# Kernel tuning notes

Hardware: AMD Instinct MI355X
Metric: run time of the kernel (lower is better)

Reference implementation:

```python
import jax, jax.numpy as jnp
import numpy as np

D = 1024
H = 16
HD = D // H


def setup_inputs() -> dict:
    key = jax.random.key(0)
    ks = jax.random.split(key, 9)
    s = 1.0 / np.sqrt(D)
    x = jax.random.normal(ks[0], (2, 2048, D), dtype=jnp.float32)
    Wq = jax.random.uniform(ks[1], (D, D), jnp.float32, -s, s)
    bq = jax.random.uniform(ks[2], (D,), jnp.float32, -s, s)
    Wk = jax.random.uniform(ks[3], (D, D), jnp.float32, -s, s)
    bk = jax.random.uniform(ks[4], (D,), jnp.float32, -s, s)
    Wv = jax.random.uniform(ks[5], (D, D), jnp.float32, -s, s)
    bv = jax.random.uniform(ks[6], (D,), jnp.float32, -s, s)
    Wo = jax.random.uniform(ks[7], (D, D), jnp.float32, -s, s)
    bo = jax.random.uniform(ks[8], (D,), jnp.float32, -s, s)
    return {"x": x, "Wq": Wq, "bq": bq, "Wk": Wk, "bk": bk,
            "Wv": Wv, "bv": bv, "Wo": Wo, "bo": bo}


def reference(x, Wq, bq, Wk, bk, Wv, bv, Wo, bo):
    B, S, _ = x.shape
    # project and split heads -> [B, H, S, HD]
    def split(t):
        return t.reshape(B, S, H, HD).transpose(0, 2, 1, 3)
    q = split(x @ Wq + bq)
    k = split(x @ Wk + bk)
    v = split(x @ Wv + bv)
    scores = jnp.einsum('bhqd,bhkd->bhqk', q, k) / np.sqrt(HD).astype(np.float32)
    attn = jax.nn.softmax(scores, axis=-1)
    ctx = jnp.einsum('bhqk,bhkd->bhqd', attn, v)  # [B,H,S,HD]
    ctx = ctx.transpose(0, 2, 1, 3).reshape(B, S, D)
    return ctx @ Wo + bo
```

## Files before the change

### kernel.cpp

```cpp
#include <hip/hip_runtime.h>
#include <hip/hip_bf16.h>
#include <math.h>

#define BB 2
#define SS 2048
#define DD 1024
#define HH 16
#define HD 64
#define MM (BB * SS)
#define NT (SS / 64)

typedef __bf16 bf16;
typedef __attribute__((ext_vector_type(8))) __bf16 bf16x8;
typedef __attribute__((ext_vector_type(4))) __bf16 bf16x4;
typedef __attribute__((ext_vector_type(4))) float f32x4;
typedef __attribute__((ext_vector_type(4))) unsigned u32x4;

#define QSCL 0.18033688011112042f

__device__ __forceinline__ void glds16(const bf16* g, bf16* l) {
    __builtin_amdgcn_global_load_lds(
        (const __attribute__((address_space(1))) void*)g,
        (__attribute__((address_space(3))) void*)l, 16, 0, 0);
}

__device__ __forceinline__ unsigned cvtpk_bf16(float a, float b) {
    unsigned r;
    asm("v_cvt_pk_bf16_f32 %0, %1, %2" : "=v"(r) : "v"(a), "v"(b));
    return r;
}

__device__ __forceinline__ float exp2p(float s) {
    float n = rintf(s);
    float f = s - n;
    float p = fmaf(f, 0.00961812910f, 0.0555041087f);
    p = fmaf(f, p, 0.240226507f);
    p = fmaf(f, p, 0.693147180f);
    p = fmaf(f, p, 1.0f);
    return ldexpf(p, (int)n);
}

__global__ __launch_bounds__(256) void cvt_prep(
    const float* __restrict__ x, bf16* __restrict__ xb,
    const float* __restrict__ W0, const float* __restrict__ W1,
    const float* __restrict__ W2, const float* __restrict__ W3,
    bf16* __restrict__ Wt) {
    __shared__ float T[64][65];
    const int bid = blockIdx.x;
    if (bid < 4096) {
        int i = (bid * 256 + threadIdx.x) * 4;
        float4 v = *(const float4*)(x + i);
        bf16x4 o;
        o[0] = (bf16)v.x; o[1] = (bf16)v.y; o[2] = (bf16)v.z; o[3] = (bf16)v.w;
        *(bf16x4*)(xb + i) = o;
        return;
    }
    const int b = bid - 4096;
    const int z = b >> 8;
    const float* W = (z == 0) ? W0 : (z == 1) ? W1 : (z == 2) ? W2 : W3;
    bf16* dst = Wt + (size_t)z * DD * DD;
    int k0 = ((b >> 4) & 15) * 64, n0 = (b & 15) * 64;
    int tr = threadIdx.x >> 4, tc = (threadIdx.x & 15) * 4;
#pragma unroll
    for (int u = 0; u < 4; u++) {
        int r = tr + u * 16;
        float4 v = *(const float4*)&W[(size_t)(k0 + r) * DD + n0 + tc];
        T[tc + 0][r] = v.x; T[tc + 1][r] = v.y;
        T[tc + 2][r] = v.z; T[tc + 3][r] = v.w;
    }
    __syncthreads();
#pragma unroll
    for (int u = 0; u < 4; u++) {
        int r = tr + u * 16;
        bf16x4 o;
        o[0] = (bf16)T[r][tc + 0]; o[1] = (bf16)T[r][tc + 1];
        o[2] = (bf16)T[r][tc + 2]; o[3] = (bf16)T[r][tc + 3];
        *(bf16x4*)&dst[(size_t)(n0 + r) * DD + k0 + tc] = o;
    }
}

__global__ __launch_bounds__(256) void mfma_gemm(
    const bf16* __restrict__ A, const bf16* __restrict__ Wt0,
    const float* __restrict__ b0, const float* __restrict__ b1,
    const float* __restrict__ b2,
    bf16* __restrict__ o0, bf16* __restrict__ o1, bf16* __restrict__ o2) {
    const int lin = blockIdx.x;
    const int nl = (lin & 7) * 96 + (lin >> 3);
    const int z = nl >> 8;
    const int rem = nl & 255;
    const int m0 = (rem >> 3) * 128;
    const int n0 = (rem & 7) * 128;

    const bf16* Wt = Wt0 + (size_t)z * DD * DD;
    const float* bias = (z == 0) ? b0 : (z == 1) ? b1 : b2;
    const float scl = (z == 0) ? QSCL : 1.0f;

    __shared__ __align__(16) bf16 As[128 * 64];
    __shared__ __align__(16) bf16 Bs[128 * 64];

    const int tid = threadIdx.x;
    const int lane = tid & 63;
    const int w = tid >> 6;
    const int l15 = lane & 15, quad = lane >> 4;
    const int mw = (w & 1) * 64;
    const int nw = (w >> 1) * 64;

    f32x4 acc[4][4];
#pragma unroll
    for (int i = 0; i < 4; i++)
#pragma unroll
        for (int j = 0; j < 4; j++) acc[i][j] = (f32x4){0.f, 0.f, 0.f, 0.f};

    for (int kt = 0; kt < DD; kt += 64) {
        __syncthreads();
#pragma unroll
        for (int u = 0; u < 4; u++) {
            int j = tid + u * 256;
            int row = j >> 3, cp = j & 7;
            int c = cp ^ (row & 7);
            glds16(A  + (size_t)(m0 + row) * DD + kt + c * 8, &As[j * 8]);
            glds16(Wt + (size_t)(n0 + row) * DD + kt + c * 8, &Bs[j * 8]);
        }
        __syncthreads();

#pragma unroll
        for (int kh = 0; kh < 2; kh++) {
            bf16x8 af[4], bf[4];
#pragma unroll
            for (int i = 0; i < 4; i++) {
                int ra = mw + i * 16 + l15;
                int ja = ra * 8 + ((kh * 4 + quad) ^ (ra & 7));
                af[i] = *(const bf16x8*)&As[ja * 8];
                int rb = nw + i * 16 + l15;
                int jb = rb * 8 + ((kh * 4 + quad) ^ (rb & 7));
                bf[i] = *(const bf16x8*)&Bs[jb * 8];
            }
#pragma unroll
            for (int i = 0; i < 4; i++)
#pragma unroll
                for (int j = 0; j < 4; j++)
                    acc[i][j] = __builtin_amdgcn_mfma_f32_16x16x32_bf16(
                        af[i], bf[j], acc[i][j], 0, 0, 0);
        }
    }

    float bcol[4];
#pragma unroll
    for (int j = 0; j < 4; j++) bcol[j] = bias[n0 + nw + j * 16 + l15];

    if (z == 2) {
        const int mbase = m0 + mw;
        const int bb = (mbase >= SS) ? 1 : 0;
        const int sw = mbase & (SS - 1);
#pragma unroll
        for (int i = 0; i < 4; i++) {
            int scol = sw + (i >> 1) * 32 + quad * 8 + (i & 1) * 4;
#pragma unroll
            for (int j = 0; j < 4; j++) {
                int dg = n0 + nw + j * 16 + l15;
                int h = dg >> 6, d = dg & 63;
                bf16* dst = o2 + ((size_t)(bb * HH + h) * HD + d) * SS + scol;
                bf16x4 ov;
#pragma unroll
                for (int r = 0; r < 4; r++)
                    ov[r] = (bf16)(acc[i][j][r] + bcol[j]);
                *(bf16x4*)dst = ov;
            }
        }
    } else {
        bf16* dstb = (z == 0) ? o0 : o1;
#pragma unroll
        for (int i = 0; i < 4; i++)
#pragma unroll
            for (int j = 0; j < 4; j++)
#pragma unroll
                for (int r = 0; r < 4; r++) {
                    int row = m0 + mw + i * 16 + quad * 4 + r;
                    int col = n0 + nw + j * 16 + l15;
                    dstb[(size_t)row * DD + col] =
                        (bf16)((acc[i][j][r] + bcol[j]) * scl);
                }
    }
}

__global__ __launch_bounds__(256) void mfma_gemm_out(
    const bf16* __restrict__ A, const bf16* __restrict__ Wt,
    const float* __restrict__ bias, float* __restrict__ out) {
    const int lin = blockIdx.x;
    const int nl = (lin & 7) * 64 + (lin >> 3);
    const int m0 = (nl >> 3) * 64;
    const int n0 = (nl & 7) * 128;

    __shared__ __align__(16) bf16 As[64 * 64];
    __shared__ __align__(16) bf16 Bs[128 * 64];

    const int tid = threadIdx.x;
    const int lane = tid & 63;
    const int w = tid >> 6;
    const int l15 = lane & 15, quad = lane >> 4;
    const int mw = (w & 1) * 32;
    const int nw = (w >> 1) * 64;

    f32x4 acc[2][4];
#pragma unroll
    for (int i = 0; i < 2; i++)
#pragma unroll
        for (int j = 0; j < 4; j++) acc[i][j] = (f32x4){0.f, 0.f, 0.f, 0.f};

    for (int kt = 0; kt < DD; kt += 64) {
        __syncthreads();
#pragma unroll
        for (int u = 0; u < 2; u++) {
            int j = tid + u * 256;
            int row = j >> 3, c = (j & 7) ^ (row & 7);
            glds16(A + (size_t)(m0 + row) * DD + kt + c * 8, &As[j * 8]);
        }
#pragma unroll
        for (int u = 0; u < 4; u++) {
            int j = tid + u * 256;
            int row = j >> 3, c = (j & 7) ^ (row & 7);
            glds16(Wt + (size_t)(n0 + row) * DD + kt + c * 8, &Bs[j * 8]);
        }
        __syncthreads();

#pragma unroll
        for (int kh = 0; kh < 2; kh++) {
            bf16x8 af[2], bf[4];
#pragma unroll
            for (int i = 0; i < 2; i++) {
                int ra = mw + i * 16 + l15;
                int ja = ra * 8 + ((kh * 4 + quad) ^ (ra & 7));
                af[i] = *(const bf16x8*)&As[ja * 8];
            }
#pragma unroll
            for (int j = 0; j < 4; j++) {
                int rb = nw + j * 16 + l15;
                int jb = rb * 8 + ((kh * 4 + quad) ^ (rb & 7));
                bf[j] = *(const bf16x8*)&Bs[jb * 8];
            }
#pragma unroll
            for (int i = 0; i < 2; i++)
#pragma unroll
                for (int j = 0; j < 4; j++)
                    acc[i][j] = __builtin_amdgcn_mfma_f32_16x16x32_bf16(
                        af[i], bf[j], acc[i][j], 0, 0, 0);
        }
    }

    float bcol[4];
#pragma unroll
    for (int j = 0; j < 4; j++) bcol[j] = bias[n0 + nw + j * 16 + l15];

#pragma unroll
    for (int i = 0; i < 2; i++)
#pragma unroll
        for (int j = 0; j < 4; j++)
#pragma unroll
            for (int r = 0; r < 4; r++) {
                int row = m0 + mw + i * 16 + quad * 4 + r;
                int col = n0 + nw + j * 16 + l15;
                out[(size_t)row * DD + col] = acc[i][j][r] + bcol[j];
            }
}

__global__ __launch_bounds__(256) void mfma_attn(
    const bf16* __restrict__ Qb, const bf16* __restrict__ Kb,
    const bf16* __restrict__ Vtg, bf16* __restrict__ ctxb) {
    __shared__ __align__(16) bf16 Ks[2][64 * 64];
    __shared__ __align__(16) bf16 Vs[2][64 * 64];

    const int lin = blockIdx.x;
    const int nl = (lin & 7) * 128 + (lin >> 3);
    const int bh = nl >> 5;
    const int q0 = (nl & 31) * 64;

    const int tid = threadIdx.x;
    const int lane = tid & 63;
    const int w = tid >> 6;
    const int l15 = lane & 15, quad = lane >> 4;
    const int b = bh >> 4, h = bh & 15;
    const size_t mb = (size_t)b * SS;
    const int hc = h * HD;
    const bf16* Vt_bh = Vtg + (size_t)bh * HD * SS;

    bf16x8 qf[2];
#pragma unroll
    for (int kh = 0; kh < 2; kh++)
        qf[kh] = *(const bf16x8*)&Qb[(mb + q0 + w * 16 + l15) * DD +
                                     hc + kh * 32 + quad * 8];

    bf16x8 onev;
#pragma unroll
    for (int i = 0; i < 8; i++) onev[i] = (bf16)1.0f;
    const f32x4 zf = (f32x4){0.f, 0.f, 0.f, 0.f};

    int koff[4][2], voff[4][2];
#pragma unroll
    for (int kb = 0; kb < 4; kb++) {
        int rk = kb * 16 + l15;
#pragma unroll
        for (int kh = 0; kh < 2; kh++)
            koff[kb][kh] = (rk * 8 + ((kh * 4 + quad) ^ (rk & 7))) * 8;
    }
#pragma unroll
    for (int nb = 0; nb < 4; nb++) {
        int rv = nb * 16 + l15;
#pragma unroll
        for (int kh = 0; kh < 2; kh++)
            voff[nb][kh] = (rv * 8 + ((kh * 4 + quad) ^ (rv & 7))) * 8;
    }

    const bf16* gK[2]; const bf16* gV[2]; int lo_[2];
#pragma unroll
    for (int u = 0; u < 2; u++) {
        int j = tid + u * 256;
        int row = j >> 3, cp = j & 7;
        int c = cp ^ (row & 7);
        gK[u] = Kb + (mb + row) * DD + hc + c * 8;
        gV[u] = Vt_bh + (size_t)row * SS + c * 8;
        lo_[u] = j * 8;
    }

    f32x4 o[4], lsum;
    lsum = (f32x4){0.f, 0.f, 0.f, 0.f};
#pragma unroll
    for (int nb = 0; nb < 4; nb++) o[nb] = (f32x4){0.f, 0.f, 0.f, 0.f};

#pragma unroll
    for (int u = 0; u < 2; u++) {
        glds16(gK[u], &Ks[0][lo_[u]]);  gK[u] += 64 * DD;
        glds16(gV[u], &Vs[0][lo_[u]]);  gV[u] += 64;
    }
    __syncthreads();

    f32x4 scA[4];
#pragma unroll
    for (int kb = 0; kb < 4; kb++) {
        bf16x8 kf0 = *(const bf16x8*)&Ks[0][koff[kb][0]];
        bf16x8 kf1 = *(const bf16x8*)&Ks[0][koff[kb][1]];
        f32x4 t = __builtin_amdgcn_mfma_f32_16x16x32_bf16(
            kf0, qf[0], zf, 0, 0, 0);
        scA[kb] = __builtin_amdgcn_mfma_f32_16x16x32_bf16(
            kf1, qf[1], t, 0, 0, 0);
    }

    int buf = 0;
    for (int it = 0; it < NT; ++it) {
        const bool more = (it + 1 < NT);
        if (more) {
#pragma unroll
            for (int u = 0; u < 2; u++) {
                glds16(gK[u], &Ks[buf ^ 1][lo_[u]]);  gK[u] += 64 * DD;
                glds16(gV[u], &Vs[buf ^ 1][lo_[u]]);  gV[u] += 64;
            }
        }

        u32x4 pw[2];
#pragma unroll
        for (int kb = 0; kb < 4; kb++) {
            float p0 = exp2p(scA[kb][0]);
            float p1 = exp2p(scA[kb][1]);
            float p2 = exp2p(scA[kb][2]);
            float p3 = exp2p(scA[kb][3]);
            pw[kb >> 1][(kb & 1) * 2 + 0] = cvtpk_bf16(p0, p1);
            pw[kb >> 1][(kb & 1) * 2 + 1] = cvtpk_bf16(p2, p3);
        }
        bf16x8 pfr[2];
        pfr[0] = __builtin_bit_cast(bf16x8, pw[0]);
        pfr[1] = __builtin_bit_cast(bf16x8, pw[1]);

        __syncthreads();

        __builtin_amdgcn_s_setprio(1);
        f32x4 scB[4];
        if (more) {
#pragma unroll
            for (int kb = 0; kb < 4; kb++) {
                bf16x8 kf0 = *(const bf16x8*)&Ks[buf ^ 1][koff[kb][0]];
                bf16x8 kf1 = *(const bf16x8*)&Ks[buf ^ 1][koff[kb][1]];
                f32x4 t = __builtin_amdgcn_mfma_f32_16x16x32_bf16(
                    kf0, qf[0], zf, 0, 0, 0);
                scB[kb] = __builtin_amdgcn_mfma_f32_16x16x32_bf16(
                    kf1, qf[1], t, 0, 0, 0);
            }
        }
#pragma unroll
        for (int kh = 0; kh < 2; kh++) {
            lsum = __builtin_amdgcn_mfma_f32_16x16x32_bf16(
                pfr[kh], onev, lsum, 0, 0, 0);
#pragma unroll
            for (int nb = 0; nb < 4; nb++) {
                bf16x8 vf = *(const bf16x8*)&Vs[buf][voff[nb][kh]];
                o[nb] = __builtin_amdgcn_mfma_f32_16x16x32_bf16(
                    pfr[kh], vf, o[nb], 0, 0, 0);
            }
        }
        __builtin_amdgcn_s_setprio(0);

        __syncthreads();

        if (more) {
#pragma unroll
            for (int kb = 0; kb < 4; kb++) scA[kb] = scB[kb];
        }
        buf ^= 1;
    }

    float li[4];
#pragma unroll
    for (int r = 0; r < 4; r++) li[r] = 1.0f / lsum[r];
#pragma unroll
    for (int nb = 0; nb < 4; nb++)
#pragma unroll
        for (int r = 0; r < 4; r++) {
            int qrow = q0 + w * 16 + quad * 4 + r;
            ctxb[(mb + qrow) * DD + hc + nb * 16 + l15] =
                (bf16)(o[nb][r] * li[r]);
        }
}

extern "C" void kernel_launch(void* const* d_in, const int* in_sizes, int n_in,
                              void* d_out, int out_size, void* d_ws, size_t ws_size,
                              hipStream_t stream) {
    const float* x  = (const float*)d_in[0];
    const float* Wq = (const float*)d_in[1];
    const float* bq = (const float*)d_in[2];
    const float* Wk = (const float*)d_in[3];
    const float* bk = (const float*)d_in[4];
    const float* Wv = (const float*)d_in[5];
    const float* bv = (const float*)d_in[6];
    const float* Wo = (const float*)d_in[7];
    const float* bo = (const float*)d_in[8];
    float* out = (float*)d_out;

    char* base = (char*)d_ws;
    bf16* xb   = (bf16*)(base);
    bf16* Wt   = (bf16*)(base + (8ull  << 20));
    bf16* Qb   = (bf16*)(base + (16ull << 20));
    bf16* Kb   = (bf16*)(base + (24ull << 20));
    bf16* Vt   = (bf16*)(base + (32ull << 20));
    bf16* ctxb = (bf16*)(base + (40ull << 20));

    cvt_prep<<<dim3(4096 + 1024), dim3(256), 0, stream>>>(
        x, xb, Wq, Wk, Wv, Wo, Wt);

    mfma_gemm<<<dim3(768), dim3(256), 0, stream>>>(
        xb, Wt, bq, bk, bv, Qb, Kb, Vt);

    mfma_attn<<<dim3(1024), dim3(256), 0, stream>>>(Qb, Kb, Vt, ctxb);

    mfma_gemm_out<<<dim3(512), dim3(256), 0, stream>>>(
        ctxb, Wt + 3ull * DD * DD, bo, out);
}
```

Measured before the change: 208.4 us.

## Rework QKV GEMM into 256x256 tiles with double-buffered LDS prefetch

The fused QKV projection GEMM moves from 128x128 tiles with 256 threads to 256x256 tiles with 512 threads, each wave computing a 128x64 sub-tile. LDS is double-buffered so the next K-slice is loaded with global_load_lds while MFMAs run on the current one, with one barrier per iteration instead of two. The MFMA section also runs at raised wave priority. The grid drops to 192 blocks, under one wave of blocks across the CUs, and the 128 KB of LDS plus larger accumulators may limit occupancy.

Result: faster. 203.7 us (median of 2 runs) (-2.2%).

```diff
diff --git a/kernel.cpp b/kernel.cpp
--- a/kernel.cpp
+++ b/kernel.cpp
@@ -79,85 +79,106 @@
     }
 }
 
-__global__ __launch_bounds__(256) void mfma_gemm(
+__global__ __launch_bounds__(512, 2) void mfma_gemm_qkv(
     const bf16* __restrict__ A, const bf16* __restrict__ Wt0,
     const float* __restrict__ b0, const float* __restrict__ b1,
     const float* __restrict__ b2,
     bf16* __restrict__ o0, bf16* __restrict__ o1, bf16* __restrict__ o2) {
+    __shared__ __align__(16) bf16 As[2][256 * 64];
+    __shared__ __align__(16) bf16 Bs[2][256 * 64];
+
     const int lin = blockIdx.x;
-    const int nl = (lin & 7) * 96 + (lin >> 3);
-    const int z = nl >> 8;
-    const int rem = nl & 255;
-    const int m0 = (rem >> 3) * 128;
-    const int n0 = (rem & 7) * 128;
-
-    const bf16* Wt = Wt0 + (size_t)z * DD * DD;
+    const int nl = (lin & 7) * 24 + (lin >> 3);
+    const int mt = nl & 15;
+    const int nt = nl >> 4;
+    const int m0 = mt * 256;
+    const int n0g = nt * 256;
+    const int z = n0g >> 10;
+    const int n0 = n0g & 1023;
+    const bf16* Wt = Wt0 + (size_t)z * DD * DD + (size_t)n0 * DD;
     const float* bias = (z == 0) ? b0 : (z == 1) ? b1 : b2;
     const float scl = (z == 0) ? QSCL : 1.0f;
-
-    __shared__ __align__(16) bf16 As[128 * 64];
-    __shared__ __align__(16) bf16 Bs[128 * 64];
 
     const int tid = threadIdx.x;
     const int lane = tid & 63;
     const int w = tid >> 6;
+    const int wm = w >> 2;
+    const int wn = w & 3;
     const int l15 = lane & 15, quad = lane >> 4;
-    const int mw = (w & 1) * 64;
-    const int nw = (w >> 1) * 64;
-
-    f32x4 acc[4][4];
-#pragma unroll
-    for (int i = 0; i < 4; i++)
+
+    const bf16* gA[4]; const bf16* gB[4]; int loff[4];
+#pragma unroll
+    for (int u = 0; u < 4; u++) {
+        int j = tid + u * 512;
+        int r = j >> 3, cp = j & 7;
+        int c = cp ^ (r & 7);
+        gA[u] = A  + (size_t)(m0 + r) * DD + c * 8;
+        gB[u] = Wt + (size_t)r * DD + c * 8;
+        loff[u] = j * 8;
+    }
+
+    f32x4 acc[8][4];
+#pragma unroll
+    for (int i = 0; i < 8; i++)
 #pragma unroll
         for (int j = 0; j < 4; j++) acc[i][j] = (f32x4){0.f, 0.f, 0.f, 0.f};
 
-    for (int kt = 0; kt < DD; kt += 64) {
-        __syncthreads();
-#pragma unroll
-        for (int u = 0; u < 4; u++) {
-            int j = tid + u * 256;
-            int row = j >> 3, cp = j & 7;
-            int c = cp ^ (row & 7);
-            glds16(A  + (size_t)(m0 + row) * DD + kt + c * 8, &As[j * 8]);
-            glds16(Wt + (size_t)(n0 + row) * DD + kt + c * 8, &Bs[j * 8]);
-        }
-        __syncthreads();
-
+#pragma unroll
+    for (int u = 0; u < 4; u++) {
+        glds16(gA[u], &As[0][loff[u]]);  gA[u] += 64;
+        glds16(gB[u], &Bs[0][loff[u]]);  gB[u] += 64;
+    }
+    __syncthreads();
+
+    for (int t = 0; t < DD / 64; ++t) {
+        const int buf = t & 1;
+        if (t + 1 < DD / 64) {
+#pragma unroll
+            for (int u = 0; u < 4; u++) {
+                glds16(gA[u], &As[buf ^ 1][loff[u]]);  gA[u] += 64;
+                glds16(gB[u], &Bs[buf ^ 1][loff[u]]);  gB[u] += 64;
+            }
+        }
+        __builtin_amdgcn_s_setprio(1);
 #pragma unroll
         for (int kh = 0; kh < 2; kh++) {
-            bf16x8 af[4], bf[4];
-#pragma unroll
-            for (int i = 0; i < 4; i++) {
-                int ra = mw + i * 16 + l15;
-                int ja = ra * 8 + ((kh * 4 + quad) ^ (ra & 7));
-                af[i] = *(const bf16x8*)&As[ja * 8];
-                int rb = nw + i * 16 + l15;
-                int jb = rb * 8 + ((kh * 4 + quad) ^ (rb & 7));
-                bf[i] = *(const bf16x8*)&Bs[jb * 8];
-            }
-#pragma unroll
-            for (int i = 0; i < 4; i++)
+            bf16x8 bfr[4];
+#pragma unroll
+            for (int j = 0; j < 4; j++) {
+                int rb = wn * 64 + j * 16 + l15;
+                bfr[j] = *(const bf16x8*)
+                    &Bs[buf][rb * 64 + (((kh * 4 + quad) ^ (rb & 7)) << 3)];
+            }
+#pragma unroll
+            for (int i = 0; i < 8; i++) {
+                int ra = wm * 128 + i * 16 + l15;
+                bf16x8 afr = *(const bf16x8*)
+                    &As[buf][ra * 64 + (((kh * 4 + quad) ^ (ra & 7)) << 3)];
 #pragma unroll
                 for (int j = 0; j < 4; j++)
                     acc[i][j] = __builtin_amdgcn_mfma_f32_16x16x32_bf16(
-                        af[i], bf[j], acc[i][j], 0, 0, 0);
-        }
+                        afr, bfr[j], acc[i][j], 0, 0, 0);
+            }
+        }
+        __builtin_amdgcn_s_setprio(0);
+        __syncthreads();
     }
 
     float bcol[4];
 #pragma unroll
-    for (int j = 0; j < 4; j++) bcol[j] = bias[n0 + nw + j * 16 + l15];
+    for (int j = 0; j < 4; j++) bcol[j] = bias[n0 + wn * 64 + j * 16 + l15];
 
     if (z == 2) {
-        const int mbase = m0 + mw;
-        const int bb = (mbase >= SS) ? 1 : 0;
-        const int sw = mbase & (SS - 1);
-#pragma unroll
-        for (int i = 0; i < 4; i++) {
-            int scol = sw + (i >> 1) * 32 + quad * 8 + (i & 1) * 4;
+#pragma unroll
+        for (int i = 0; i < 8; i++) {
+            const int g = i >> 2, ig = i & 3;
+            const int mb64 = m0 + wm * 128 + g * 64;
+            const int bb = (mb64 >= SS) ? 1 : 0;
+            const int sw = mb64 & (SS - 1);
+            const int scol = sw + (ig >> 1) * 32 + quad * 8 + (ig & 1) * 4;
 #pragma unroll
             for (int j = 0; j < 4; j++) {
-                int dg = n0 + nw + j * 16 + l15;
+                int dg = n0 + wn * 64 + j * 16 + l15;
                 int h = dg >> 6, d = dg & 63;
                 bf16* dst = o2 + ((size_t)(bb * HH + h) * HD + d) * SS + scol;
                 bf16x4 ov;
@@ -170,13 +191,13 @@
     } else {
         bf16* dstb = (z == 0) ? o0 : o1;
 #pragma unroll
-        for (int i = 0; i < 4; i++)
+        for (int i = 0; i < 8; i++)
 #pragma unroll
             for (int j = 0; j < 4; j++)
 #pragma unroll
                 for (int r = 0; r < 4; r++) {
-                    int row = m0 + mw + i * 16 + quad * 4 + r;
-                    int col = n0 + nw + j * 16 + l15;
+                    int row = m0 + wm * 128 + i * 16 + quad * 4 + r;
+                    int col = n0 + wn * 64 + j * 16 + l15;
                     dstb[(size_t)row * DD + col] =
                         (bf16)((acc[i][j][r] + bcol[j]) * scl);
                 }
@@ -444,7 +465,7 @@
     cvt_prep<<<dim3(4096 + 1024), dim3(256), 0, stream>>>(
         x, xb, Wq, Wk, Wv, Wo, Wt);
 
-    mfma_gemm<<<dim3(768), dim3(256), 0, stream>>>(
+    mfma_gemm_qkv<<<dim3(192), dim3(512), 0, stream>>>(
         xb, Wt, bq, bk, bv, Qb, Kb, Vt);
 
     mfma_attn<<<dim3(1024), dim3(256), 0, stream>>>(Qb, Kb, Vt, ctxb);
```
